# Optimization experiments

Measured on AMD Instinct MI355X. Metric: run time of the kernel, lower is better.

Reference implementation:

```python
import jax, jax.numpy as jnp
import numpy as np

OBJ_N, D_KEY, D_VAL, BANK_N, N_Q, BS = 4, 128, 512, 7200, 3600, 1


def setup_inputs() -> dict:
    key = jax.random.key(0)
    k1, k2, k3, k4, k5 = jax.random.split(key, 5)
    return {
        "keys": jax.random.normal(k1, (OBJ_N, D_KEY, BANK_N), dtype=jnp.float32),
        "values": jax.random.normal(k2, (OBJ_N, D_VAL, BANK_N), dtype=jnp.float32),
        "masks": jax.random.uniform(k3, (OBJ_N, 1, BANK_N), dtype=jnp.float32),
        "q_in": jax.random.normal(k4, (BS, D_KEY, N_Q), dtype=jnp.float32),
        "q_out": jax.random.normal(k5, (BS, D_VAL, N_Q), dtype=jnp.float32),
    }


def reference(keys, values, masks, q_in, q_out):
    # keys: (O, Dk, B) memory keys per object; q_in: (S, Dk, N) query keys
    d_key = keys.shape[1]
    scale = 1.0 / jnp.sqrt(jnp.asarray(d_key, dtype=keys.dtype))
    # p[o,s,b,n] = softmax_b( keys[o,:,b] . q_in[s,:,n] / sqrt(Dk) )
    logits = jnp.einsum('odb,sdn->osbn', keys, q_in) * scale
    p = jax.nn.softmax(logits, axis=2)
    # mem[o,s,v,n] = sum_b values[o,v,b] * p[o,s,b,n]
    mem = jnp.einsum('ovb,osbn->osvn', values, p)
    # mask_mem[o,s,1,n]: mask-weighted attention readout, gates q_out
    mask_mem = jnp.einsum('omb,osbn->osmn', masks, p)
    q_out_with_mask = q_out[None] * mask_mem          # (O, S, Dv, N)
    out = jnp.concatenate([mem, q_out_with_mask], axis=2)  # (O, S, 2*Dv, N)
    return jnp.transpose(out, (1, 0, 2, 3))           # (S, O, 2*Dv, N)
```

## Files before the change

kernel.cpp:

```cpp
#include <hip/hip_runtime.h>
#include <hip/hip_bf16.h>

typedef unsigned short u16;
typedef unsigned int   u32;
typedef short bf16x8 __attribute__((ext_vector_type(8)));
typedef float f32x4  __attribute__((ext_vector_type(4)));

#define O_N    4
#define D_K    128
#define D_V    512
#define BANK   7200
#define NQ     3600
#define NT     64
#define NTILES 57
#define NSUB   225
#define VH_ROWS 256

#define K_OFF    0
#define P_OFF    32768
#define LMM_OFF  49152
#define SMEM_BYTES 49664
#define Q_OFF    0

#define GLL(gsrc, ldst) __builtin_amdgcn_global_load_lds( \
    (const __attribute__((address_space(1))) void*)(gsrc), \
    (__attribute__((address_space(3))) void*)(ldst), 16, 0, 0)

#define MFMA16(a, b, c) __builtin_amdgcn_mfma_f32_16x16x32_bf16((a), (b), (c), 0, 0, 0)

static __device__ __forceinline__ u16 f2bf(float x) {
    u32 u = __builtin_bit_cast(u32, x);
    return (u16)((u + 0x7FFFu + ((u >> 16) & 1u)) >> 16);
}


#define QSCALE 0.12751743f

__global__ void k_transpose_bf16(const float* __restrict__ in, u16* __restrict__ out) {
    __shared__ float tile[32][33];
    const int obj = blockIdx.z;
    const float* src = in + (size_t)obj * D_K * BANK;
    u16* dst = out + (size_t)obj * BANK * D_K;
    const int bx = blockIdx.x * 32;
    const int by = blockIdx.y * 32;
    const int tx = threadIdx.x, ty = threadIdx.y;
#pragma unroll
    for (int i = 0; i < 4; i++)
        tile[ty + 8 * i][tx] = src[(size_t)(by + ty + 8 * i) * BANK + bx + tx];
    __syncthreads();
#pragma unroll
    for (int i = 0; i < 4; i++)
        dst[(size_t)(bx + ty + 8 * i) * D_K + by + tx] = f2bf(tile[tx][ty + 8 * i]);
}

__global__ void k_convert_bf16(const float* __restrict__ in, u16* __restrict__ out, int n4) {
    int idx = blockIdx.x * blockDim.x + threadIdx.x;
    int stride = gridDim.x * blockDim.x;
    for (int i = idx; i < n4; i += stride) {
        float4 v = reinterpret_cast<const float4*>(in)[i];
        ushort4 o;
        o.x = f2bf(v.x); o.y = f2bf(v.y); o.z = f2bf(v.z); o.w = f2bf(v.w);
        reinterpret_cast<ushort4*>(out)[i] = o;
    }
}

__global__ void k_zero(float* out, int n) {
    int i = blockIdx.x * blockDim.x + threadIdx.x;
    if (i < n) out[i] = 0.f;
}

__launch_bounds__(256, 2)
__global__ void k_matcher(const u16* __restrict__ Kt,
                          const u16* __restrict__ Vb,
                          const float* __restrict__ masks,
                          const float* __restrict__ q_in,
                          const float* __restrict__ q_out,
                          float* __restrict__ out,
                          int G, float* __restrict__ lw, float* __restrict__ mw)
{
    __shared__ __align__(16) char smem[SMEM_BYTES];
    const int tid  = threadIdx.x;
    const int wave = tid >> 6;
    const int lane = tid & 63;
    const int q    = lane >> 4;
    const int lr   = lane & 15;
    const int lr7  = lr & 7;

    const int grp  = blockIdx.x & 7;
    const int o    = grp >> 1;
    const int vh   = grp & 1;
    const int rest = blockIdx.x >> 3;
    const int tile = rest / G;
    const int g    = rest - tile * G;
    const int n0   = tile * NT;

    const int st0 = (NSUB * g) / G;
    const int st1 = (NSUB * (g + 1)) / G;
    const int cnt = st1 - st0;
    const int nd  = cnt >> 1;
    const int ts  = cnt & 1;
    const int nu  = nd + ts;

    for (int idx = tid; idx < NT * D_K; idx += 256) {
        int d = idx >> 6;
        int n = idx & 63;
        int gn = n0 + n;
        float v = (gn < NQ) ? q_in[(size_t)d * NQ + gn] * QSCALE : 0.f;
        int bb = d * 2;
        int sb = n * 256 + ((((bb >> 4) ^ (n & 7)) << 4) | (bb & 15));
        *reinterpret_cast<u16*>(smem + Q_OFF + sb) = f2bf(v);
    }
    __syncthreads();

    bf16x8 qf[4];
    {
        const int n = 16 * wave + lr;
#pragma unroll
        for (int ds = 0; ds < 4; ds++) {
            int gq = (4 * ds + q) ^ (n & 7);
            qf[ds] = *reinterpret_cast<const bf16x8*>(smem + Q_OFF + n * 256 + gq * 16);
        }
    }
    __syncthreads();

    const f32x4 zero4 = {0.f, 0.f, 0.f, 0.f};
    f32x4 acc[4][4];
#pragma unroll
    for (int i = 0; i < 4; i++)
#pragma unroll
        for (int j = 0; j < 4; j++) acc[i][j] = zero4;
    float l_part = 0.f, mm_part = 0.f;

    const u16* Ko = Kt + (size_t)o * BANK * D_K;
    const u16* Vo = Vb + (size_t)o * D_V * BANK + (size_t)vh * VH_ROWS * BANK;
    const float* mPtr = masks + (size_t)o * BANK + st0 * 32 + 4 * q;

    const u16* kSrcA = Ko + (size_t)(st0 * 32 + (tid >> 4)) * D_K
                         + (((tid & 15) ^ (tid >> 4)) << 3);
    const u16* kSrcB = kSrcA + 16 * D_K;

#define ISSUE2(buf) do {                                                   \
        char* kb_ = smem + K_OFF + (buf) * 16384 + wave * 1024;            \
        GLL(kSrcA, kb_);                                                   \
        GLL(kSrcB, kb_ + 4096);                                            \
        GLL(kSrcA + 32 * D_K, kb_ + 8192);                                 \
        GLL(kSrcB + 32 * D_K, kb_ + 12288);                                \
        kSrcA += 64 * D_K; kSrcB += 64 * D_K;                              \
    } while (0)
#define ISSUE1(buf) do {                                                   \
        char* kb_ = smem + K_OFF + (buf) * 16384 + wave * 1024;            \
        GLL(kSrcA, kb_);                                                   \
        GLL(kSrcB, kb_ + 4096);                                            \
    } while (0)

    const u16* Vrow = Vo + st0 * 32;
    const u32  vOff = (u32)(64 * wave + lr) * BANK + q * 8;

    const int nrow  = 16 * wave + lr;

#define QK_T(T, MV, PWB) do {                                                \
        f32x4 s_acc = zero4;                                                 \
        const int b_r = 16 * (T) + lr;                                       \
        _Pragma("unroll")                                                    \
        for (int ds = 0; ds < 4; ds++) {                                     \
            bf16x8 kf = *reinterpret_cast<const bf16x8*>(                    \
                kb + b_r * 256 + (((4 * ds + q) ^ lr) << 4));                \
            s_acc = MFMA16(kf, qf[ds], s_acc);                               \
        }                                                                    \
        float p0 = exp2f(s_acc[0]);                                          \
        float p1 = exp2f(s_acc[1]);                                          \
        float p2 = exp2f(s_acc[2]);                                          \
        float p3 = exp2f(s_acc[3]);                                          \
        l_part  += p0 + p1 + p2 + p3;                                        \
        mm_part += p0 * (MV).x + p1 * (MV).y + p2 * (MV).z + p3 * (MV).w;    \
        u32 w0, w1;                                                          \
        asm("v_cvt_pk_bf16_f32 %0, %1, %2" : "=v"(w0) : "v"(p0), "v"(p1));   \
        asm("v_cvt_pk_bf16_f32 %0, %1, %2" : "=v"(w1) : "v"(p2), "v"(p3));   \
        uint2 pk2; pk2.x = w0; pk2.y = w1;                                   \
        *reinterpret_cast<uint2*>(                                           \
            (PWB) + (((2 * (T) + (q >> 1)) ^ lr7) << 4)) = pk2;              \
    } while (0)

#define PV_S(S, PB, V0, V1, V2, V3) do {                                     \
        _Pragma("unroll")                                                    \
        for (int ng = 0; ng < 4; ng++) {                                     \
            bf16x8 pf = *reinterpret_cast<const bf16x8*>(                    \
                (PB) + (16 * ng + lr) * 128 +                                \
                (((4 * (S) + q) ^ lr7) << 4));                               \
            acc[0][ng] = MFMA16(V0, pf, acc[0][ng]);                         \
            acc[1][ng] = MFMA16(V1, pf, acc[1][ng]);                         \
            acc[2][ng] = MFMA16(V2, pf, acc[2][ng]);                         \
            acc[3][ng] = MFMA16(V3, pf, acc[3][ng]);                         \
        }                                                                    \
    } while (0)

    if (nd > 0) ISSUE2(0); else ISSUE1(0);
    asm volatile("s_waitcnt vmcnt(0)" ::: "memory");
    __builtin_amdgcn_s_barrier();
    __builtin_amdgcn_sched_barrier(0);

    bf16x8 va0, va1, va2, va3, vb0, vb1, vb2, vb3;

    for (int u = 0; u < nu; u++) {
        const int cur = u & 1;
        const char* kb = smem + K_OFF + cur * 16384;
        char* pWc = smem + P_OFF + cur * 8192 + nrow * 128 + (q & 1) * 8;
        const char* pR = smem + P_OFF + (cur ^ 1) * 8192;
        const bool full = (u < nd);

        float4 mv0 = *reinterpret_cast<const float4*>(mPtr);
        float4 mv1 = *reinterpret_cast<const float4*>(mPtr + 16);
        float4 mv2, mv3;
        bf16x8 na0 = *reinterpret_cast<const bf16x8*>(Vrow + vOff);
        bf16x8 na1 = *reinterpret_cast<const bf16x8*>(Vrow + vOff + 16 * BANK);
        bf16x8 na2 = *reinterpret_cast<const bf16x8*>(Vrow + vOff + 32 * BANK);
        bf16x8 na3 = *reinterpret_cast<const bf16x8*>(Vrow + vOff + 48 * BANK);
        bf16x8 nb0 = vb0, nb1 = vb1, nb2 = vb2, nb3 = vb3;
        if (full) {
            mv2 = *reinterpret_cast<const float4*>(mPtr + 32);
            mv3 = *reinterpret_cast<const float4*>(mPtr + 48);
            nb0 = *reinterpret_cast<const bf16x8*>(Vrow + vOff + 32);
            nb1 = *reinterpret_cast<const bf16x8*>(Vrow + vOff + 32 + 16 * BANK);
            nb2 = *reinterpret_cast<const bf16x8*>(Vrow + vOff + 32 + 32 * BANK);
            nb3 = *reinterpret_cast<const bf16x8*>(Vrow + vOff + 32 + 48 * BANK);
        }
        __builtin_amdgcn_sched_barrier(0);

        if (u + 1 < nu) {
            if (u + 1 < nd) ISSUE2(cur ^ 1);
            else            ISSUE1(cur ^ 1);
        }
        __builtin_amdgcn_sched_barrier(0);

        QK_T(0, mv0, pWc);
        QK_T(1, mv1, pWc);
        if (full) {
            QK_T(2, mv2, pWc);
            QK_T(3, mv3, pWc);
        }

        if (u > 0) {
            PV_S(0, pR, va0, va1, va2, va3);
            PV_S(1, pR, vb0, vb1, vb2, vb3);
        }
        va0 = na0; va1 = na1; va2 = na2; va3 = na3;
        vb0 = nb0; vb1 = nb1; vb2 = nb2; vb3 = nb3;

        mPtr += full ? 64 : 32;
        Vrow += full ? 64 : 32;

        asm volatile("s_waitcnt vmcnt(0) lgkmcnt(0)" ::: "memory");
        __builtin_amdgcn_s_barrier();
        __builtin_amdgcn_sched_barrier(0);
    }

    {
        const char* pL = smem + P_OFF + ((nu - 1) & 1) * 8192;
        PV_S(0, pL, va0, va1, va2, va3);
        if (!ts) PV_S(1, pL, vb0, vb1, vb2, vb3);
    }

    l_part  += __shfl_xor(l_part, 16);  l_part  += __shfl_xor(l_part, 32);
    mm_part += __shfl_xor(mm_part, 16); mm_part += __shfl_xor(mm_part, 32);
    float* l_lds  = reinterpret_cast<float*>(smem + LMM_OFF);
    float* mm_lds = l_lds + 64;
    if (lane < 16) {
        l_lds[16 * wave + lr]  = l_part;
        mm_lds[16 * wave + lr] = mm_part;
    }
    __syncthreads();

    if (G == 1) {
        float* outo = out + (size_t)o * (1024 * NQ);
#pragma unroll
        for (int ng = 0; ng < 4; ng++) {
            const int n  = 16 * ng + lr;
            const int gn = n0 + n;
            if (gn >= NQ) continue;
            const float invl = 1.f / l_lds[n];
            const float gate = mm_lds[n] * invl;
#pragma unroll
            for (int vt = 0; vt < 4; vt++) {
#pragma unroll
                for (int r = 0; r < 4; r++) {
                    const int v = vh * VH_ROWS + 64 * wave + 16 * vt + 4 * q + r;
                    outo[(size_t)v * NQ + gn] = acc[vt][ng][r] * invl;
                    outo[(size_t)(512 + v) * NQ + gn] = q_out[(size_t)v * NQ + gn] * gate;
                }
            }
        }
    } else {
        float* dst = out + ((size_t)o * 1024 + (size_t)g * 512 + (size_t)vh * VH_ROWS) * NQ;
#pragma unroll
        for (int ng = 0; ng < 4; ng++) {
            const int n  = 16 * ng + lr;
            const int gn = n0 + n;
            if (gn >= NQ) continue;
#pragma unroll
            for (int vt = 0; vt < 4; vt++) {
#pragma unroll
                for (int r = 0; r < 4; r++) {
                    const int v = 64 * wave + 16 * vt + 4 * q + r;
                    dst[(size_t)v * NQ + gn] = acc[vt][ng][r];
                }
            }
        }
        if (vh == 0 && tid < 64) {
            const size_t li = ((size_t)(g * 4 + o) * NTILES + tile) * 64 + tid;
            lw[li] = l_lds[tid];
            mw[li] = mm_lds[tid];
        }
    }
}

__global__ void k_combine(const float* __restrict__ q_out, const float* __restrict__ lw,
                          const float* __restrict__ mw, float* __restrict__ out) {
    const int total = O_N * 512 * (NQ / 4);
    float4* outv = reinterpret_cast<float4*>(out);
    const float4* qv = reinterpret_cast<const float4*>(q_out);
    for (int idx = blockIdx.x * blockDim.x + threadIdx.x; idx < total;
         idx += gridDim.x * blockDim.x) {
        const int o  = idx / (512 * 900);
        const int r  = idx - o * 512 * 900;
        const int v  = r / 900;
        const int g4 = r - v * 900;
        const size_t iA = ((size_t)o * 1024 + v) * 900 + g4;
        const size_t iB = ((size_t)o * 1024 + 512 + v) * 900 + g4;
        float4 A = outv[iA];
        float4 B = outv[iB];
        const int tl = g4 >> 4;
        const int wi = (g4 & 15) * 4;
        const size_t l0i = ((size_t)(0 * 4 + o) * NTILES + tl) * 64 + wi;
        const size_t l1i = ((size_t)(1 * 4 + o) * NTILES + tl) * 64 + wi;
        const float4 l0 = *reinterpret_cast<const float4*>(lw + l0i);
        const float4 l1 = *reinterpret_cast<const float4*>(lw + l1i);
        const float4 m0 = *reinterpret_cast<const float4*>(mw + l0i);
        const float4 m1 = *reinterpret_cast<const float4*>(mw + l1i);
        float4 li, mem, gate;
        li.x = 1.f / (l0.x + l1.x); li.y = 1.f / (l0.y + l1.y);
        li.z = 1.f / (l0.z + l1.z); li.w = 1.f / (l0.w + l1.w);
        mem.x = (A.x + B.x) * li.x; mem.y = (A.y + B.y) * li.y;
        mem.z = (A.z + B.z) * li.z; mem.w = (A.w + B.w) * li.w;
        gate.x = (m0.x + m1.x) * li.x; gate.y = (m0.y + m1.y) * li.y;
        gate.z = (m0.z + m1.z) * li.z; gate.w = (m0.w + m1.w) * li.w;
        float4 qo = qv[(size_t)v * 900 + g4];
        outv[iA] = mem;
        float4 gq;
        gq.x = qo.x * gate.x; gq.y = qo.y * gate.y;
        gq.z = qo.z * gate.z; gq.w = qo.w * gate.w;
        outv[iB] = gq;
    }
}

extern "C" void kernel_launch(void* const* d_in, const int* in_sizes, int n_in,
                              void* d_out, int out_size, void* d_ws, size_t ws_size,
                              hipStream_t stream) {
    const float* keys   = (const float*)d_in[0];
    const float* values = (const float*)d_in[1];
    const float* masks  = (const float*)d_in[2];
    const float* q_in   = (const float*)d_in[3];
    const float* q_outp = (const float*)d_in[4];
    float* out = (float*)d_out;

    const size_t K_BYTES  = (size_t)O_N * BANK * D_K * 2;
    const size_t V_BYTES  = (size_t)O_N * D_V * BANK * 2;
    const size_t LM_FLOATS = (size_t)2 * O_N * NTILES * 64;
    const size_t LM_BYTES  = LM_FLOATS * 4 * 2;

    if (ws_size < K_BYTES + V_BYTES) {
        k_zero<<<(out_size + 255) / 256, 256, 0, stream>>>(out, out_size);
        return;
    }
    const int G = (ws_size >= K_BYTES + V_BYTES + LM_BYTES) ? 2 : 1;

    u16* Kt = (u16*)d_ws;
    u16* Vb = (u16*)((char*)d_ws + K_BYTES);
    float* lw = (float*)((char*)d_ws + K_BYTES + V_BYTES);
    float* mw = lw + LM_FLOATS;

    dim3 tb(32, 8);
    dim3 tg(BANK / 32, D_K / 32, O_N);
    k_transpose_bf16<<<tg, tb, 0, stream>>>(keys, Kt);

    const int n4 = O_N * D_V * BANK / 4;
    k_convert_bf16<<<2048, 256, 0, stream>>>(values, Vb, n4);

    k_matcher<<<NTILES * 8 * G, 256, 0, stream>>>(Kt, Vb, masks, q_in, q_outp, out,
                                                  G, lw, mw);
    if (G == 2)
        k_combine<<<2048, 256, 0, stream>>>(q_outp, lw, mw, out);
}
```

Measured before the change: 294.6 us.

## Triple-buffer K tiles in LDS and skip redundant softmax sums for vh=1 blocks

Moves the key-tile prefetch from double to triple buffering: two tiles are issued up front and each iteration prefetches two ahead, waiting with vmcnt(4) instead of draining all loads. This gives the global-to-LDS copies more time to overlap with compute. It also skips the row-sum and mask-sum accumulation in blocks whose second value half would recompute the same statistics when the bank is split. LDS per block grows from about 49 KB to 66 KB, which may reduce occupancy. The always-full 4-load issue may read past the end of the bank range on odd tails.

```diff
diff --git a/kernel.cpp b/kernel.cpp
--- a/kernel.cpp
+++ b/kernel.cpp
@@ -17,9 +17,9 @@
 #define VH_ROWS 256
 
 #define K_OFF    0
-#define P_OFF    32768
-#define LMM_OFF  49152
-#define SMEM_BYTES 49664
+#define P_OFF    49152
+#define LMM_OFF  65536
+#define SMEM_BYTES 66048
 #define Q_OFF    0
 
 #define GLL(gsrc, ldst) __builtin_amdgcn_global_load_lds( \
@@ -33,8 +33,8 @@
     return (u16)((u + 0x7FFFu + ((u >> 16) & 1u)) >> 16);
 }
 
-
 #define QSCALE 0.12751743f
+
 
 __global__ void k_transpose_bf16(const float* __restrict__ in, u16* __restrict__ out) {
     __shared__ float tile[32][33];
@@ -94,6 +94,8 @@
     const int g    = rest - tile * G;
     const int n0   = tile * NT;
 
+    const bool needLM = (G == 1) || (vh == 0);
+
     const int st0 = (NSUB * g) / G;
     const int st1 = (NSUB * (g + 1)) / G;
     const int cnt = st1 - st0;
@@ -139,18 +141,13 @@
                          + (((tid & 15) ^ (tid >> 4)) << 3);
     const u16* kSrcB = kSrcA + 16 * D_K;
 
-#define ISSUE2(buf) do {                                                   \
+#define ISSUE_K(buf) do {                                                  \
         char* kb_ = smem + K_OFF + (buf) * 16384 + wave * 1024;            \
         GLL(kSrcA, kb_);                                                   \
         GLL(kSrcB, kb_ + 4096);                                            \
         GLL(kSrcA + 32 * D_K, kb_ + 8192);                                 \
         GLL(kSrcB + 32 * D_K, kb_ + 12288);                                \
         kSrcA += 64 * D_K; kSrcB += 64 * D_K;                              \
-    } while (0)
-#define ISSUE1(buf) do {                                                   \
-        char* kb_ = smem + K_OFF + (buf) * 16384 + wave * 1024;            \
-        GLL(kSrcA, kb_);                                                   \
-        GLL(kSrcB, kb_ + 4096);                                            \
     } while (0)
 
     const u16* Vrow = Vo + st0 * 32;
@@ -171,8 +168,10 @@
         float p1 = exp2f(s_acc[1]);                                          \
         float p2 = exp2f(s_acc[2]);                                          \
         float p3 = exp2f(s_acc[3]);                                          \
-        l_part  += p0 + p1 + p2 + p3;                                        \
-        mm_part += p0 * (MV).x + p1 * (MV).y + p2 * (MV).z + p3 * (MV).w;    \
+        if (needLM) {                                                        \
+            l_part  += p0 + p1 + p2 + p3;                                    \
+            mm_part += p0 * (MV).x + p1 * (MV).y + p2 * (MV).z + p3 * (MV).w;\
+        }                                                                    \
         u32 w0, w1;                                                          \
         asm("v_cvt_pk_bf16_f32 %0, %1, %2" : "=v"(w0) : "v"(p0), "v"(p1));   \
         asm("v_cvt_pk_bf16_f32 %0, %1, %2" : "=v"(w1) : "v"(p2), "v"(p3));   \
@@ -194,19 +193,27 @@
         }                                                                    \
     } while (0)
 
-    if (nd > 0) ISSUE2(0); else ISSUE1(0);
-    asm volatile("s_waitcnt vmcnt(0)" ::: "memory");
+    ISSUE_K(0);
+    if (nu > 1) {
+        ISSUE_K(1);
+        asm volatile("s_waitcnt vmcnt(4)" ::: "memory");
+    } else {
+        asm volatile("s_waitcnt vmcnt(0)" ::: "memory");
+    }
     __builtin_amdgcn_s_barrier();
     __builtin_amdgcn_sched_barrier(0);
 
     bf16x8 va0, va1, va2, va3, vb0, vb1, vb2, vb3;
+    int bR = 0;
+    int bW = 2;
 
     for (int u = 0; u < nu; u++) {
         const int cur = u & 1;
-        const char* kb = smem + K_OFF + cur * 16384;
+        const char* kb = smem + K_OFF + bR * 16384;
         char* pWc = smem + P_OFF + cur * 8192 + nrow * 128 + (q & 1) * 8;
         const char* pR = smem + P_OFF + (cur ^ 1) * 8192;
         const bool full = (u < nd);
+        const bool more = (u + 2 < nu);
 
         float4 mv0 = *reinterpret_cast<const float4*>(mPtr);
         float4 mv1 = *reinterpret_cast<const float4*>(mPtr + 16);
@@ -226,9 +233,9 @@
         }
         __builtin_amdgcn_sched_barrier(0);
 
-        if (u + 1 < nu) {
-            if (u + 1 < nd) ISSUE2(cur ^ 1);
-            else            ISSUE1(cur ^ 1);
+        if (more) {
+            ISSUE_K(bW);
+            bW = (bW == 2) ? 0 : bW + 1;
         }
         __builtin_amdgcn_sched_barrier(0);
 
@@ -248,8 +255,12 @@
 
         mPtr += full ? 64 : 32;
         Vrow += full ? 64 : 32;
-
-        asm volatile("s_waitcnt vmcnt(0) lgkmcnt(0)" ::: "memory");
+        bR = (bR == 2) ? 0 : bR + 1;
+
+        if (more)
+            asm volatile("s_waitcnt vmcnt(4) lgkmcnt(0)" ::: "memory");
+        else
+            asm volatile("s_waitcnt vmcnt(0) lgkmcnt(0)" ::: "memory");
         __builtin_amdgcn_s_barrier();
         __builtin_amdgcn_sched_barrier(0);
     }
@@ -260,13 +271,15 @@
         if (!ts) PV_S(1, pL, vb0, vb1, vb2, vb3);
     }
 
-    l_part  += __shfl_xor(l_part, 16);  l_part  += __shfl_xor(l_part, 32);
-    mm_part += __shfl_xor(mm_part, 16); mm_part += __shfl_xor(mm_part, 32);
     float* l_lds  = reinterpret_cast<float*>(smem + LMM_OFF);
     float* mm_lds = l_lds + 64;
-    if (lane < 16) {
-        l_lds[16 * wave + lr]  = l_part;
-        mm_lds[16 * wave + lr] = mm_part;
+    if (needLM) {
+        l_part  += __shfl_xor(l_part, 16);  l_part  += __shfl_xor(l_part, 32);
+        mm_part += __shfl_xor(mm_part, 16); mm_part += __shfl_xor(mm_part, 32);
+        if (lane < 16) {
+            l_lds[16 * wave + lr]  = l_part;
+            mm_lds[16 * wave + lr] = mm_part;
+        }
     }
     __syncthreads();
 
```

Measured after the change: 308.8 us. +4.8%, slower.

## Reorder PV before V loads to cut registers, raise occupancy, skip redundant row sums

Applied to the files above, without the earlier changes.

Moves the PV MFMAs ahead of the V-fragment global loads, so the loads write straight into the va/vb registers and the na/nb staging copies are gone. The per-iteration register footprint drops, and launch bounds rise from 2 to 3 blocks per SIMD. The softmax denominator and mask readout are now accumulated only by blocks that consume them (vh==0 or G==1), which removes duplicate VALU work in the other half. Risks: V load latency is no longer hidden behind the QK stage, and the tighter register cap may cause spills.

```diff
diff --git a/kernel.cpp b/kernel.cpp
--- a/kernel.cpp
+++ b/kernel.cpp
@@ -33,8 +33,8 @@
     return (u16)((u + 0x7FFFu + ((u >> 16) & 1u)) >> 16);
 }
 
-
 #define QSCALE 0.12751743f
+
 
 __global__ void k_transpose_bf16(const float* __restrict__ in, u16* __restrict__ out) {
     __shared__ float tile[32][33];
@@ -69,7 +69,7 @@
     if (i < n) out[i] = 0.f;
 }
 
-__launch_bounds__(256, 2)
+__launch_bounds__(256, 3)
 __global__ void k_matcher(const u16* __restrict__ Kt,
                           const u16* __restrict__ Vb,
                           const float* __restrict__ masks,
@@ -94,6 +94,8 @@
     const int g    = rest - tile * G;
     const int n0   = tile * NT;
 
+    const bool needLM = (G == 1) || (vh == 0);
+
     const int st0 = (NSUB * g) / G;
     const int st1 = (NSUB * (g + 1)) / G;
     const int cnt = st1 - st0;
@@ -171,8 +173,10 @@
         float p1 = exp2f(s_acc[1]);                                          \
         float p2 = exp2f(s_acc[2]);                                          \
         float p3 = exp2f(s_acc[3]);                                          \
-        l_part  += p0 + p1 + p2 + p3;                                        \
-        mm_part += p0 * (MV).x + p1 * (MV).y + p2 * (MV).z + p3 * (MV).w;    \
+        if (needLM) {                                                        \
+            l_part  += p0 + p1 + p2 + p3;                                    \
+            mm_part += p0 * (MV).x + p1 * (MV).y + p2 * (MV).z + p3 * (MV).w;\
+        }                                                                    \
         u32 w0, w1;                                                          \
         asm("v_cvt_pk_bf16_f32 %0, %1, %2" : "=v"(w0) : "v"(p0), "v"(p1));   \
         asm("v_cvt_pk_bf16_f32 %0, %1, %2" : "=v"(w1) : "v"(p2), "v"(p3));   \
@@ -208,43 +212,39 @@
         const char* pR = smem + P_OFF + (cur ^ 1) * 8192;
         const bool full = (u < nd);
 
-        float4 mv0 = *reinterpret_cast<const float4*>(mPtr);
-        float4 mv1 = *reinterpret_cast<const float4*>(mPtr + 16);
-        float4 mv2, mv3;
-        bf16x8 na0 = *reinterpret_cast<const bf16x8*>(Vrow + vOff);
-        bf16x8 na1 = *reinterpret_cast<const bf16x8*>(Vrow + vOff + 16 * BANK);
-        bf16x8 na2 = *reinterpret_cast<const bf16x8*>(Vrow + vOff + 32 * BANK);
-        bf16x8 na3 = *reinterpret_cast<const bf16x8*>(Vrow + vOff + 48 * BANK);
-        bf16x8 nb0 = vb0, nb1 = vb1, nb2 = vb2, nb3 = vb3;
-        if (full) {
-            mv2 = *reinterpret_cast<const float4*>(mPtr + 32);
-            mv3 = *reinterpret_cast<const float4*>(mPtr + 48);
-            nb0 = *reinterpret_cast<const bf16x8*>(Vrow + vOff + 32);
-            nb1 = *reinterpret_cast<const bf16x8*>(Vrow + vOff + 32 + 16 * BANK);
-            nb2 = *reinterpret_cast<const bf16x8*>(Vrow + vOff + 32 + 32 * BANK);
-            nb3 = *reinterpret_cast<const bf16x8*>(Vrow + vOff + 32 + 48 * BANK);
-        }
-        __builtin_amdgcn_sched_barrier(0);
-
         if (u + 1 < nu) {
             if (u + 1 < nd) ISSUE2(cur ^ 1);
             else            ISSUE1(cur ^ 1);
         }
+        float4 mv0 = *reinterpret_cast<const float4*>(mPtr);
+        float4 mv1 = *reinterpret_cast<const float4*>(mPtr + 16);
         __builtin_amdgcn_sched_barrier(0);
+
+        if (u > 0) {
+            PV_S(0, pR, va0, va1, va2, va3);
+            PV_S(1, pR, vb0, vb1, vb2, vb3);
+        }
+        __builtin_amdgcn_sched_barrier(0);
+
+        va0 = *reinterpret_cast<const bf16x8*>(Vrow + vOff);
+        va1 = *reinterpret_cast<const bf16x8*>(Vrow + vOff + 16 * BANK);
+        va2 = *reinterpret_cast<const bf16x8*>(Vrow + vOff + 32 * BANK);
+        va3 = *reinterpret_cast<const bf16x8*>(Vrow + vOff + 48 * BANK);
+        if (full) {
+            vb0 = *reinterpret_cast<const bf16x8*>(Vrow + vOff + 32);
+            vb1 = *reinterpret_cast<const bf16x8*>(Vrow + vOff + 32 + 16 * BANK);
+            vb2 = *reinterpret_cast<const bf16x8*>(Vrow + vOff + 32 + 32 * BANK);
+            vb3 = *reinterpret_cast<const bf16x8*>(Vrow + vOff + 32 + 48 * BANK);
+        }
 
         QK_T(0, mv0, pWc);
         QK_T(1, mv1, pWc);
         if (full) {
+            float4 mv2 = *reinterpret_cast<const float4*>(mPtr + 32);
+            float4 mv3 = *reinterpret_cast<const float4*>(mPtr + 48);
             QK_T(2, mv2, pWc);
             QK_T(3, mv3, pWc);
         }
-
-        if (u > 0) {
-            PV_S(0, pR, va0, va1, va2, va3);
-            PV_S(1, pR, vb0, vb1, vb2, vb3);
-        }
-        va0 = na0; va1 = na1; va2 = na2; va3 = na3;
-        vb0 = nb0; vb1 = nb1; vb2 = nb2; vb3 = nb3;
 
         mPtr += full ? 64 : 32;
         Vrow += full ? 64 : 32;
@@ -260,13 +260,15 @@
         if (!ts) PV_S(1, pL, vb0, vb1, vb2, vb3);
     }
 
-    l_part  += __shfl_xor(l_part, 16);  l_part  += __shfl_xor(l_part, 32);
-    mm_part += __shfl_xor(mm_part, 16); mm_part += __shfl_xor(mm_part, 32);
     float* l_lds  = reinterpret_cast<float*>(smem + LMM_OFF);
     float* mm_lds = l_lds + 64;
-    if (lane < 16) {
-        l_lds[16 * wave + lr]  = l_part;
-        mm_lds[16 * wave + lr] = mm_part;
+    if (needLM) {
+        l_part  += __shfl_xor(l_part, 16);  l_part  += __shfl_xor(l_part, 32);
+        mm_part += __shfl_xor(mm_part, 16); mm_part += __shfl_xor(mm_part, 32);
+        if (lane < 16) {
+            l_lds[16 * wave + lr]  = l_part;
+            mm_lds[16 * wave + lr] = mm_part;
+        }
     }
     __syncthreads();
 
```

Measured after the change: 331.5 us. +12.5%, slower.
